# Kernel optimization log

Measured on AMD Instinct MI355X. Metric: run time of the kernel, lower is better.

## Reference

```python
import jax, jax.numpy as jnp
import numpy as np

DIM = 512
NUM_HEADS = 8
HEAD_DIM = DIM // NUM_HEADS
SCALE = HEAD_DIM ** -0.5


def setup_inputs() -> dict:
    key = jax.random.key(0)
    ks = jax.random.split(key, 5)
    B, D, H, W, C = 2, 8, 16, 16, DIM
    x = jax.random.normal(ks[0], (B, D, H, W, C), dtype=jnp.float32)
    # torch Linear params stored as [in, out] so y = x @ W + b
    qkv_w = jax.random.normal(ks[1], (C, 3 * C), dtype=jnp.float32) * (C ** -0.5)
    qkv_b = jax.random.normal(ks[2], (3 * C,), dtype=jnp.float32) * 0.02
    proj_w = jax.random.normal(ks[3], (C, C), dtype=jnp.float32) * (C ** -0.5)
    proj_b = jax.random.normal(ks[4], (C,), dtype=jnp.float32) * 0.02
    return {"x": x, "qkv_w": qkv_w, "qkv_b": qkv_b, "proj_w": proj_w, "proj_b": proj_b}


def reference(x, qkv_w, qkv_b, proj_w, proj_b):
    B, D, H, W, C = x.shape
    N = D * H * W
    x_flat = x.reshape(B, N, C)
    qkv = (x_flat @ qkv_w + qkv_b).reshape(B, N, 3, NUM_HEADS, HEAD_DIM)
    qkv = jnp.transpose(qkv, (2, 0, 3, 1, 4))  # [3, B, h, N, hd]
    q, k, v = qkv[0], qkv[1], qkv[2]
    attn = jnp.einsum('bhnd,bhmd->bhnm', q, k) * SCALE  # [B, h, N, N]
    attn = jnp.clip(attn, -10000.0, 10000.0)
    attn = jax.nn.softmax(attn, axis=-1)
    attn = jnp.nan_to_num(attn, nan=0.0)
    out = jnp.einsum('bhnm,bhmd->bhnd', attn, v)  # [B, h, N, hd]
    out = jnp.transpose(out, (0, 2, 1, 3)).reshape(B, N, C)
    out = out @ proj_w + proj_b
    return out.reshape(B, D, H, W, C)
```

## Files before the change

### kernel.cpp

```cpp
#include <hip/hip_runtime.h>
#include <stdint.h>

typedef unsigned short u16;
typedef __bf16 bf16x8 __attribute__((ext_vector_type(8)));
typedef __bf16 bf16x4 __attribute__((ext_vector_type(4)));
typedef _Float16 f16x4 __attribute__((ext_vector_type(4)));
typedef _Float16 f16x8 __attribute__((ext_vector_type(8)));
typedef float  f32x4  __attribute__((ext_vector_type(4)));

__device__ __forceinline__ u16 f2bf(float f) {
  union { float f; unsigned u; } v; v.f = f;
  unsigned r = v.u + 0x7FFFu + ((v.u >> 16) & 1u);
  return (u16)(r >> 16);
}

__device__ __forceinline__ void gload16(const void* g, void* l) {
  __builtin_amdgcn_global_load_lds((const __attribute__((address_space(1))) unsigned int*)g,
                                   (__attribute__((address_space(3))) unsigned int*)l, 16, 0, 0);
}

__device__ __forceinline__ f32x4 mfma32(bf16x8 a, bf16x8 b, f32x4 c) {
  return __builtin_amdgcn_mfma_f32_16x16x32_bf16(a, b, c, 0, 0, 0);
}

__global__ void k_prep(const float* __restrict__ x, const float* __restrict__ qw,
                       const float* __restrict__ pjw, u16* __restrict__ Xb,
                       u16* __restrict__ Wt, u16* __restrict__ Pt) {
  __shared__ u16 tile[64][65];
  const int b = blockIdx.x, t = threadIdx.x;
  if (b < 2048) {
    int i = b * 256 + t;
    float4 v = ((const float4*)x)[i];
    uint2 o;
    o.x = (unsigned)f2bf(v.x) | ((unsigned)f2bf(v.y) << 16);
    o.y = (unsigned)f2bf(v.z) | ((unsigned)f2bf(v.w) << 16);
    ((uint2*)Xb)[i] = o;
    return;
  }
  const float* in; u16* out; int Cc, bx, by;
  if (b < 2240) { in = qw;  out = Wt; Cc = 1536; bx = (b - 2048) % 24; by = (b - 2048) / 24; }
  else          { in = pjw; out = Pt; Cc = 512;  bx = (b - 2240) & 7;  by = (b - 2240) >> 3; }
  const int c0 = bx * 64, r0 = by * 64;
  #pragma unroll
  for (int i = 0; i < 16; ++i) {
    int idx = t + i * 256;
    int r = idx >> 6, c = idx & 63;
    tile[c][r] = f2bf(in[(size_t)(r0 + r) * Cc + c0 + c]);
  }
  __syncthreads();
  #pragma unroll
  for (int i = 0; i < 16; ++i) {
    int idx = t + i * 256;
    int r = idx >> 6, c = idx & 63;
    out[(size_t)(c0 + r) * 512 + r0 + c] = tile[r][c];
  }
}

__device__ __forceinline__ int swz32(int row, int chunk) {
  return row * 32 + ((chunk ^ ((row >> 1) & 3)) << 3);
}
__device__ __forceinline__ int swz64(int row, int colByte) {
  return (row * 128 + (colByte ^ ((row & 7) << 4))) >> 1;
}
__device__ __forceinline__ int swzK(int row, int colByte) {
  return (row * 128 + (colByte ^ ((row & 3) << 4) ^ (((row >> 3) & 1) << 6))) >> 1;
}

template<int BM, int BN>
__device__ __forceinline__ void gemm_core(const u16* __restrict__ A, const u16* __restrict__ Bt,
                                          int m0, int n0, f32x4 (&acc)[BM/32][BN/32],
                                          u16* lA, u16* lB) {
  const int t = threadIdx.x;
  const int lane = t & 63;
  const int w = t >> 6, wr = w >> 1, wc = w & 1;
  const int lr = lane & 15, lg = lane >> 4;
  char* lAb = (char*)lA + w * 1024;
  char* lBb = (char*)lB + w * 1024;
  #pragma unroll 1
  for (int k0 = 0; k0 < 512; k0 += 32) {
    __syncthreads();
    #pragma unroll
    for (int u = 0; u < BM / 64; ++u) {
      int id = u * 256 + t, row = id >> 2, gc = (id & 3) ^ ((row >> 1) & 3);
      gload16(A + (size_t)(m0 + row) * 512 + k0 + gc * 8, lAb + u * 4096);
    }
    #pragma unroll
    for (int u = 0; u < BN / 64; ++u) {
      int id = u * 256 + t, row = id >> 2, gc = (id & 3) ^ ((row >> 1) & 3);
      gload16(Bt + (size_t)(n0 + row) * 512 + k0 + gc * 8, lBb + u * 4096);
    }
    __syncthreads();
    bf16x8 af[BM / 32], bfr[BN / 32];
    #pragma unroll
    for (int i = 0; i < BM / 32; ++i)
      af[i] = __builtin_bit_cast(bf16x8, *(const uint4*)&lA[swz32(wr * (BM / 2) + i * 16 + lr, lg)]);
    #pragma unroll
    for (int j = 0; j < BN / 32; ++j)
      bfr[j] = __builtin_bit_cast(bf16x8, *(const uint4*)&lB[swz32(wc * (BN / 2) + j * 16 + lr, lg)]);
    #pragma unroll
    for (int i = 0; i < BM / 32; ++i)
      #pragma unroll
      for (int j = 0; j < BN / 32; ++j)
        acc[i][j] = __builtin_amdgcn_mfma_f32_16x16x32_bf16(af[i], bfr[j], acc[i][j], 0, 0, 0);
  }
}

__global__ __launch_bounds__(256, 2) void k_gemm_qkv(const u16* __restrict__ A, const u16* __restrict__ Bt,
                                                     const float* __restrict__ bias,
                                                     u16* __restrict__ Qb, u16* __restrict__ Kb,
                                                     u16* __restrict__ Vtb) {
  __shared__ __align__(16) u16 lA[128 * 32];
  __shared__ __align__(16) u16 lB[64 * 32];
  __shared__ __align__(16) u16 vt[9216];
  f32x4 acc[4][2];
  #pragma unroll
  for (int i = 0; i < 4; ++i)
    #pragma unroll
    for (int j = 0; j < 2; ++j) acc[i][j] = (f32x4){0.f, 0.f, 0.f, 0.f};
  const int m0 = blockIdx.x * 128, n0 = blockIdx.y * 64;
  gemm_core<128, 64>(A, Bt, m0, n0, acc, lA, lB);
  const int t = threadIdx.x;
  const int lane = t & 63;
  const int w = t >> 6, wr = w >> 1, wc = w & 1;
  const int lr = lane & 15, lg = lane >> 4;
  const int which = n0 >> 9, h = (n0 >> 6) & 7;
  const int b = m0 >> 11, m0l = m0 & 2047;
  const size_t bh = (size_t)(b * 8 + h);
  if (which != 2) {
    const float scl = (which == 0) ? 0.18033688011112042f : 1.0f;
    #pragma unroll
    for (int i = 0; i < 4; ++i)
      #pragma unroll
      for (int j = 0; j < 2; ++j) {
        int n = n0 + wc * 32 + j * 16 + lr;
        float bb = bias[n];
        #pragma unroll
        for (int r = 0; r < 4; ++r)
          vt[(wr * 64 + i * 16 + lg * 4 + r) * 72 + wc * 32 + j * 16 + lr] =
              f2bf((acc[i][j][r] + bb) * scl);
      }
    __syncthreads();
    u16* dst = (which == 0 ? Qb : Kb) + (bh * 2048 + m0l) * 64;
    #pragma unroll
    for (int it = 0; it < 4; ++it) {
      int unit = it * 256 + t, row = unit >> 3, ch = unit & 7;
      *(uint4*)&dst[row * 64 + ch * 8] = *(const uint4*)&vt[row * 72 + ch * 8];
    }
  } else {
    #pragma unroll
    for (int i = 0; i < 4; ++i)
      #pragma unroll
      for (int j = 0; j < 2; ++j) {
        int n = n0 + wc * 32 + j * 16 + lr;
        float bb = bias[n];
        uint2 pk;
        pk.x = (unsigned)f2bf(acc[i][j][0] + bb) | ((unsigned)f2bf(acc[i][j][1] + bb) << 16);
        pk.y = (unsigned)f2bf(acc[i][j][2] + bb) | ((unsigned)f2bf(acc[i][j][3] + bb) << 16);
        *(uint2*)&vt[(wc * 32 + j * 16 + lr) * 136 + wr * 64 + i * 16 + lg * 4] = pk;
      }
    __syncthreads();
    u16* dst = Vtb + bh * 64 * 2048 + m0l;
    #pragma unroll
    for (int it = 0; it < 4; ++it) {
      int unit = it * 256 + t, row = unit >> 4, ch = unit & 15;
      *(uint4*)&dst[(size_t)row * 2048 + ch * 8] = *(const uint4*)&vt[row * 136 + ch * 8];
    }
  }
}

__global__ __launch_bounds__(256, 2) void k_gemm_proj(const u16* __restrict__ A, const u16* __restrict__ Bt,
                                                      const float* __restrict__ bias,
                                                      float* __restrict__ out) {
  __shared__ __align__(16) u16 lA[64 * 32];
  __shared__ __align__(16) u16 lB[64 * 32];
  f32x4 acc[2][2];
  #pragma unroll
  for (int i = 0; i < 2; ++i)
    #pragma unroll
    for (int j = 0; j < 2; ++j) acc[i][j] = (f32x4){0.f, 0.f, 0.f, 0.f};
  const int m0 = blockIdx.x * 64, n0 = blockIdx.y * 64;
  gemm_core<64, 64>(A, Bt, m0, n0, acc, lA, lB);
  const int lane = threadIdx.x & 63;
  const int w = threadIdx.x >> 6, wr = w >> 1, wc = w & 1;
  const int lr = lane & 15, lg = lane >> 4;
  #pragma unroll
  for (int i = 0; i < 2; ++i)
    #pragma unroll
    for (int j = 0; j < 2; ++j)
      #pragma unroll
      for (int r = 0; r < 4; ++r) {
        int m = m0 + wr * 32 + i * 16 + lg * 4 + r;
        int n = n0 + wc * 32 + j * 16 + lr;
        out[(size_t)m * 512 + n] = acc[i][j][r] + bias[n];
      }
}

__global__ __launch_bounds__(256, 4) void k_attn(const u16* __restrict__ Qb, const u16* __restrict__ Kb,
                                                 const u16* __restrict__ Vtb,
                                                 u16* __restrict__ Op, float* __restrict__ Lp) {
  __shared__ __align__(16) u16 smem[16384];
  u16* Kt0 = smem;
  u16* Kt1 = smem + 4096;
  u16* Vl0 = smem + 8192;
  u16* Vl1 = smem + 12288;
  const int t = threadIdx.x;
  const int lane = t & 63, w = t >> 6;
  const int lr = lane & 15, lg = lane >> 4;
  const int f = blockIdx.x;
  const int xc = f & 7, jj = f >> 3;
  const int group = xc + ((jj >> 4) << 3);
  const int qtile = jj & 15, bh = group & 15, split = group >> 4;
  const int q0 = qtile * 128 + w * 32;
  const int sBeg = split * 512;

  bf16x8 qf[2][2];
  #pragma unroll
  for (int c = 0; c < 2; ++c) {
    const u16* qrow = Qb + ((size_t)bh * 2048 + q0 + c * 16 + lr) * 64;
    qf[c][0] = __builtin_bit_cast(bf16x8, *(const uint4*)(qrow + lg * 8));
    qf[c][1] = __builtin_bit_cast(bf16x8, *(const uint4*)(qrow + 32 + lg * 8));
  }

  f32x4 oacc[2][4], lacc[2];
  #pragma unroll
  for (int c = 0; c < 2; ++c) {
    lacc[c] = (f32x4){0.f, 0.f, 0.f, 0.f};
    #pragma unroll
    for (int ff = 0; ff < 4; ++ff) oacc[c][ff] = (f32x4){0.f, 0.f, 0.f, 0.f};
  }
  bf16x8 ones8;
  #pragma unroll
  for (int k = 0; k < 8; ++k) ones8[k] = (__bf16)1.f;
  const f32x4 NEG12 = (f32x4){-12.f, -12.f, -12.f, -12.f};

  const int prowBase = ((lr >> 2) << 3) + (lr & 3);

  const int r0 = t >> 3, j0 = t & 7;
  const int r1 = r0 + 32;
  const int cK = (j0 ^ ((r0 & 3) | (((r0 >> 3) & 1) << 2))) * 8;
  const int cV = (j0 ^ (r0 & 7)) * 8;
  const u16* Kbase = Kb + (size_t)bh * 2048 * 64;
  const u16* Vbase = Vtb + (size_t)bh * 64 * 2048;
  const u16* kg0 = Kbase + (size_t)(sBeg + r0) * 64 + cK;
  const u16* kg1 = Kbase + (size_t)(sBeg + r1) * 64 + cK;
  const u16* vg0 = Vbase + (size_t)r0 * 2048 + sBeg + cV;
  const u16* vg1 = Vbase + (size_t)r1 * 2048 + sBeg + cV;

  gload16(kg0, Kt0 + w * 512);
  gload16(kg1, Kt0 + 2048 + w * 512);
  gload16(vg0, Vl0 + w * 512);
  gload16(vg1, Vl0 + 2048 + w * 512);
  kg0 += 4096; kg1 += 4096; vg0 += 64; vg1 += 64;

  auto TILE = [&](u16* KC, u16* VC, u16* KN, u16* VN) {
    __syncthreads();
    gload16(kg0, KN + w * 512);
    gload16(kg1, KN + 2048 + w * 512);
    gload16(vg0, VN + w * 512);
    gload16(vg1, VN + 2048 + w * 512);
    kg0 += 4096; kg1 += 4096; vg0 += 64; vg1 += 64;
    #pragma unroll
    for (int j32 = 0; j32 < 2; ++j32) {
      f32x4 sa[2][2];
      __builtin_amdgcn_s_setprio(1);
      #pragma unroll
      for (int p = 0; p < 2; ++p) {
        const int prow = j32 * 32 + p * 4 + prowBase;
        bf16x8 kb0 = __builtin_bit_cast(bf16x8, *(const uint4*)&KC[swzK(prow, lg * 16)]);
        bf16x8 kb1 = __builtin_bit_cast(bf16x8, *(const uint4*)&KC[swzK(prow, 64 + lg * 16)]);
        #pragma unroll
        for (int c = 0; c < 2; ++c) {
          f32x4 z = mfma32(kb0, qf[c][0], NEG12);
          sa[c][p] = mfma32(kb1, qf[c][1], z);
        }
      }
      __builtin_amdgcn_s_setprio(0);
      bf16x8 pb[2];
      #pragma unroll
      for (int c = 0; c < 2; ++c)
        #pragma unroll
        for (int p = 0; p < 2; ++p)
          #pragma unroll
          for (int r = 0; r < 4; ++r)
            pb[c][p * 4 + r] = (__bf16)exp2f(sa[c][p][r]);
      __builtin_amdgcn_s_setprio(1);
      lacc[0] = mfma32(ones8, pb[0], lacc[0]);
      lacc[1] = mfma32(ones8, pb[1], lacc[1]);
      #pragma unroll
      for (int ff = 0; ff < 4; ++ff) {
        bf16x8 va = __builtin_bit_cast(bf16x8, *(const uint4*)&VC[swz64(ff * 16 + lr, j32 * 64 + lg * 16)]);
        oacc[0][ff] = mfma32(va, pb[0], oacc[0][ff]);
        oacc[1][ff] = mfma32(va, pb[1], oacc[1][ff]);
      }
      __builtin_amdgcn_s_setprio(0);
    }
  };

  #pragma unroll 1
  for (int tt = 0; tt < 4; ++tt) {
    TILE(Kt0, Vl0, Kt1, Vl1);
    TILE(Kt1, Vl1, Kt0, Vl0);
  }

  __syncthreads();
  #pragma unroll
  for (int c = 0; c < 2; ++c) {
    const int ql = w * 32 + c * 16 + lr;
    #pragma unroll
    for (int ff = 0; ff < 4; ++ff) {
      f16x4 hv;
      hv[0] = (_Float16)oacc[c][ff][0]; hv[1] = (_Float16)oacc[c][ff][1];
      hv[2] = (_Float16)oacc[c][ff][2]; hv[3] = (_Float16)oacc[c][ff][3];
      *(uint2*)&smem[ql * 72 + ff * 16 + lg * 4] = __builtin_bit_cast(uint2, hv);
    }
  }
  __syncthreads();
  {
    u16* dst = Op + ((size_t)(split * 16 + bh) * 2048 + qtile * 128) * 64;
    #pragma unroll
    for (int it = 0; it < 4; ++it) {
      int unit = it * 256 + t, row = unit >> 3, ch = unit & 7;
      *(uint4*)&dst[row * 64 + ch * 8] = *(const uint4*)&smem[row * 72 + ch * 8];
    }
  }
  #pragma unroll
  for (int c = 0; c < 2; ++c) {
    if (lg == 0) {
      const size_t orow = (size_t)((split * 16 + bh) * 2048) + q0 + c * 16 + lr;
      Lp[orow] = lacc[c][0];
    }
  }
}

__global__ void k_combine(const u16* __restrict__ Op, const float* __restrict__ Lp,
                          u16* __restrict__ AO) {
  int idx = blockIdx.x * 256 + threadIdx.x;
  int chunk = idx & 7, row = idx >> 3;
  float den = Lp[row] + Lp[32768 + row] + Lp[65536 + row] + Lp[98304 + row];
  float inv = 1.0f / den;
  float o[8];
  #pragma unroll
  for (int k = 0; k < 8; ++k) o[k] = 0.f;
  #pragma unroll
  for (int s = 0; s < 4; ++s) {
    uint4 u = ((const uint4*)Op)[(size_t)s * 262144 + row * 8 + chunk];
    f16x8 hv = __builtin_bit_cast(f16x8, u);
    #pragma unroll
    for (int k = 0; k < 8; ++k) o[k] += (float)hv[k];
  }
  bf16x8 bv;
  #pragma unroll
  for (int k = 0; k < 8; ++k) bv[k] = (__bf16)(o[k] * inv);
  int bh = row >> 11, q = row & 2047, bb = bh >> 3, h = bh & 7;
  *(uint4*)&AO[((size_t)(bb * 2048 + q)) * 512 + h * 64 + chunk * 8] = __builtin_bit_cast(uint4, bv);
}

extern "C" void kernel_launch(void* const* d_in, const int* in_sizes, int n_in,
                              void* d_out, int out_size, void* d_ws, size_t ws_size,
                              hipStream_t stream) {
  (void)in_sizes; (void)n_in; (void)out_size; (void)ws_size;
  const float* x      = (const float*)d_in[0];
  const float* qkv_w  = (const float*)d_in[1];
  const float* qkv_b  = (const float*)d_in[2];
  const float* proj_w = (const float*)d_in[3];
  const float* proj_b = (const float*)d_in[4];
  float* out = (float*)d_out;
  char* wsc = (char*)d_ws;
  float* Lp  = (float*)(wsc + 0);
  u16*   Xb  = (u16*)(wsc + 0);
  u16*   Wt  = (u16*)(wsc + 4194304);
  u16*   Pt  = (u16*)(wsc + 5767168);
  u16*   Qb  = (u16*)(wsc + 6291456);
  u16*   Kb  = (u16*)(wsc + 10485760);
  u16*   Vtb = (u16*)(wsc + 14680064);
  u16*   AO  = (u16*)(wsc + 18874368);
  u16*   Op  = (u16*)(wsc + 23068672);

  k_prep<<<2304, 256, 0, stream>>>(x, qkv_w, proj_w, Xb, Wt, Pt);
  k_gemm_qkv<<<dim3(32, 24), 256, 0, stream>>>(Xb, Wt, qkv_b, Qb, Kb, Vtb);
  k_attn<<<1024, 256, 0, stream>>>(Qb, Kb, Vtb, Op, Lp);
  k_combine<<<1024, 256, 0, stream>>>(Op, Lp, AO);
  k_gemm_proj<<<dim3(64, 8), 256, 0, stream>>>(AO, Pt, proj_b, out);
}
```

Baseline: 63.25 us.

## Double GEMM K-step to 64 and widen attention blocks to 512 threads

Measured after the change: 60.32 us (median of 3 runs). 4.6% less time.

```diff
diff --git a/kernel.cpp b/kernel.cpp
--- a/kernel.cpp
+++ b/kernel.cpp
@@ -3,7 +3,6 @@
 
 typedef unsigned short u16;
 typedef __bf16 bf16x8 __attribute__((ext_vector_type(8)));
-typedef __bf16 bf16x4 __attribute__((ext_vector_type(4)));
 typedef _Float16 f16x4 __attribute__((ext_vector_type(4)));
 typedef _Float16 f16x8 __attribute__((ext_vector_type(8)));
 typedef float  f32x4  __attribute__((ext_vector_type(4)));
@@ -56,9 +55,6 @@
   }
 }
 
-__device__ __forceinline__ int swz32(int row, int chunk) {
-  return row * 32 + ((chunk ^ ((row >> 1) & 3)) << 3);
-}
 __device__ __forceinline__ int swz64(int row, int colByte) {
   return (row * 128 + (colByte ^ ((row & 7) << 4))) >> 1;
 }
@@ -74,34 +70,33 @@
   const int lane = t & 63;
   const int w = t >> 6, wr = w >> 1, wc = w & 1;
   const int lr = lane & 15, lg = lane >> 4;
-  char* lAb = (char*)lA + w * 1024;
-  char* lBb = (char*)lB + w * 1024;
+  const int r0 = t >> 3, j0 = t & 7;
+  const int cA = (j0 ^ (r0 & 7)) * 8;
   #pragma unroll 1
-  for (int k0 = 0; k0 < 512; k0 += 32) {
-    __syncthreads();
-    #pragma unroll
-    for (int u = 0; u < BM / 64; ++u) {
-      int id = u * 256 + t, row = id >> 2, gc = (id & 3) ^ ((row >> 1) & 3);
-      gload16(A + (size_t)(m0 + row) * 512 + k0 + gc * 8, lAb + u * 4096);
-    }
-    #pragma unroll
-    for (int u = 0; u < BN / 64; ++u) {
-      int id = u * 256 + t, row = id >> 2, gc = (id & 3) ^ ((row >> 1) & 3);
-      gload16(Bt + (size_t)(n0 + row) * 512 + k0 + gc * 8, lBb + u * 4096);
-    }
-    __syncthreads();
-    bf16x8 af[BM / 32], bfr[BN / 32];
-    #pragma unroll
-    for (int i = 0; i < BM / 32; ++i)
-      af[i] = __builtin_bit_cast(bf16x8, *(const uint4*)&lA[swz32(wr * (BM / 2) + i * 16 + lr, lg)]);
-    #pragma unroll
-    for (int j = 0; j < BN / 32; ++j)
-      bfr[j] = __builtin_bit_cast(bf16x8, *(const uint4*)&lB[swz32(wc * (BN / 2) + j * 16 + lr, lg)]);
-    #pragma unroll
-    for (int i = 0; i < BM / 32; ++i)
+  for (int k0 = 0; k0 < 512; k0 += 64) {
+    __syncthreads();
+    #pragma unroll
+    for (int u = 0; u < BM / 32; ++u)
+      gload16(A + (size_t)(m0 + u * 32 + r0) * 512 + k0 + cA, (char*)lA + u * 4096 + w * 1024);
+    #pragma unroll
+    for (int u = 0; u < BN / 32; ++u)
+      gload16(Bt + (size_t)(n0 + u * 32 + r0) * 512 + k0 + cA, (char*)lB + u * 4096 + w * 1024);
+    __syncthreads();
+    #pragma unroll
+    for (int kh = 0; kh < 2; ++kh) {
+      bf16x8 af[BM / 32], bfr[BN / 32];
+      #pragma unroll
+      for (int i = 0; i < BM / 32; ++i)
+        af[i] = __builtin_bit_cast(bf16x8, *(const uint4*)&lA[swz64(wr * (BM / 2) + i * 16 + lr, kh * 64 + lg * 16)]);
       #pragma unroll
       for (int j = 0; j < BN / 32; ++j)
-        acc[i][j] = __builtin_amdgcn_mfma_f32_16x16x32_bf16(af[i], bfr[j], acc[i][j], 0, 0, 0);
+        bfr[j] = __builtin_bit_cast(bf16x8, *(const uint4*)&lB[swz64(wc * (BN / 2) + j * 16 + lr, kh * 64 + lg * 16)]);
+      #pragma unroll
+      for (int i = 0; i < BM / 32; ++i)
+        #pragma unroll
+        for (int j = 0; j < BN / 32; ++j)
+          acc[i][j] = mfma32(af[i], bfr[j], acc[i][j]);
+    }
   }
 }
 
@@ -109,8 +104,8 @@
                                                      const float* __restrict__ bias,
                                                      u16* __restrict__ Qb, u16* __restrict__ Kb,
                                                      u16* __restrict__ Vtb) {
-  __shared__ __align__(16) u16 lA[128 * 32];
-  __shared__ __align__(16) u16 lB[64 * 32];
+  __shared__ __align__(16) u16 lA[128 * 64];
+  __shared__ __align__(16) u16 lB[64 * 64];
   __shared__ __align__(16) u16 vt[9216];
   f32x4 acc[4][2];
   #pragma unroll
@@ -171,8 +166,8 @@
 __global__ __launch_bounds__(256, 2) void k_gemm_proj(const u16* __restrict__ A, const u16* __restrict__ Bt,
                                                       const float* __restrict__ bias,
                                                       float* __restrict__ out) {
-  __shared__ __align__(16) u16 lA[64 * 32];
-  __shared__ __align__(16) u16 lB[64 * 32];
+  __shared__ __align__(16) u16 lA[64 * 64];
+  __shared__ __align__(16) u16 lB[64 * 64];
   f32x4 acc[2][2];
   #pragma unroll
   for (int i = 0; i < 2; ++i)
@@ -195,10 +190,10 @@
       }
 }
 
-__global__ __launch_bounds__(256, 4) void k_attn(const u16* __restrict__ Qb, const u16* __restrict__ Kb,
+__global__ __launch_bounds__(512, 4) void k_attn(const u16* __restrict__ Qb, const u16* __restrict__ Kb,
                                                  const u16* __restrict__ Vtb,
                                                  u16* __restrict__ Op, float* __restrict__ Lp) {
-  __shared__ __align__(16) u16 smem[16384];
+  __shared__ __align__(16) u16 smem[18432];
   u16* Kt0 = smem;
   u16* Kt1 = smem + 4096;
   u16* Vl0 = smem + 8192;
@@ -208,9 +203,9 @@
   const int lr = lane & 15, lg = lane >> 4;
   const int f = blockIdx.x;
   const int xc = f & 7, jj = f >> 3;
-  const int group = xc + ((jj >> 4) << 3);
-  const int qtile = jj & 15, bh = group & 15, split = group >> 4;
-  const int q0 = qtile * 128 + w * 32;
+  const int group = xc + ((jj >> 3) << 3);
+  const int qtile = jj & 7, bh = group & 15, split = group >> 4;
+  const int q0 = qtile * 256 + w * 32;
   const int sBeg = split * 512;
 
   bf16x8 qf[2][2];
@@ -236,29 +231,22 @@
   const int prowBase = ((lr >> 2) << 3) + (lr & 3);
 
   const int r0 = t >> 3, j0 = t & 7;
-  const int r1 = r0 + 32;
   const int cK = (j0 ^ ((r0 & 3) | (((r0 >> 3) & 1) << 2))) * 8;
   const int cV = (j0 ^ (r0 & 7)) * 8;
   const u16* Kbase = Kb + (size_t)bh * 2048 * 64;
   const u16* Vbase = Vtb + (size_t)bh * 64 * 2048;
   const u16* kg0 = Kbase + (size_t)(sBeg + r0) * 64 + cK;
-  const u16* kg1 = Kbase + (size_t)(sBeg + r1) * 64 + cK;
   const u16* vg0 = Vbase + (size_t)r0 * 2048 + sBeg + cV;
-  const u16* vg1 = Vbase + (size_t)r1 * 2048 + sBeg + cV;
 
   gload16(kg0, Kt0 + w * 512);
-  gload16(kg1, Kt0 + 2048 + w * 512);
   gload16(vg0, Vl0 + w * 512);
-  gload16(vg1, Vl0 + 2048 + w * 512);
-  kg0 += 4096; kg1 += 4096; vg0 += 64; vg1 += 64;
+  kg0 += 4096; vg0 += 64;
 
   auto TILE = [&](u16* KC, u16* VC, u16* KN, u16* VN) {
     __syncthreads();
     gload16(kg0, KN + w * 512);
-    gload16(kg1, KN + 2048 + w * 512);
     gload16(vg0, VN + w * 512);
-    gload16(vg1, VN + 2048 + w * 512);
-    kg0 += 4096; kg1 += 4096; vg0 += 64; vg1 += 64;
+    kg0 += 4096; vg0 += 64;
     #pragma unroll
     for (int j32 = 0; j32 < 2; ++j32) {
       f32x4 sa[2][2];
@@ -316,10 +304,10 @@
   }
   __syncthreads();
   {
-    u16* dst = Op + ((size_t)(split * 16 + bh) * 2048 + qtile * 128) * 64;
+    u16* dst = Op + ((size_t)(split * 16 + bh) * 2048 + qtile * 256) * 64;
     #pragma unroll
     for (int it = 0; it < 4; ++it) {
-      int unit = it * 256 + t, row = unit >> 3, ch = unit & 7;
+      int unit = it * 512 + t, row = unit >> 3, ch = unit & 7;
       *(uint4*)&dst[row * 64 + ch * 8] = *(const uint4*)&smem[row * 72 + ch * 8];
     }
   }
@@ -378,7 +366,7 @@
 
   k_prep<<<2304, 256, 0, stream>>>(x, qkv_w, proj_w, Xb, Wt, Pt);
   k_gemm_qkv<<<dim3(32, 24), 256, 0, stream>>>(Xb, Wt, qkv_b, Qb, Kb, Vtb);
-  k_attn<<<1024, 256, 0, stream>>>(Qb, Kb, Vtb, Op, Lp);
+  k_attn<<<512, 512, 0, stream>>>(Qb, Kb, Vtb, Op, Lp);
   k_combine<<<1024, 256, 0, stream>>>(Op, Lp, AO);
   k_gemm_proj<<<dim3(64, 8), 256, 0, stream>>>(AO, Pt, proj_b, out);
 }
```
